# Kernel optimization log

Hardware: AMD Instinct MI355X
Metric: run time of the kernel (lower is better)

## Reference

```python
import jax, jax.numpy as jnp
import numpy as np

B, L, VOCAB = 32768, 512, 50000
CROP_RATIO, MIN_LEN = 0.8, 3
MASK_RATIO, MASK_TOKEN = 0.2, 0
REORDER_RATIO, MIN_W, MAX_W = 0.3, 2, 5


def setup_inputs() -> dict:
    key = jax.random.key(0)
    k1, k2 = jax.random.split(key)
    lens = jax.random.randint(k1, (B,), 1, L + 1)
    items = jax.random.randint(k2, (B, L), 1, VOCAB)
    pos = jnp.arange(L)[None, :]
    item_seq = jnp.where(pos < lens[:, None], items, 0).astype(jnp.int32)
    return {"item_seq": item_seq, "item_seq_len": lens.astype(jnp.int32)}


def _mask_aug(key, seq, lens):
    pos = jnp.arange(seq.shape[1])[None, :]
    valid = (pos < lens[:, None]) & (seq != 0)
    n_valid = valid.sum(axis=1)
    n_mask = jnp.minimum(jnp.maximum(1, (n_valid * MASK_RATIO).astype(jnp.int32)), n_valid)
    scores = jnp.where(valid, jax.random.uniform(key, seq.shape), jnp.inf)
    # rank of each position among valid positions by random score
    rank = jnp.argsort(jnp.argsort(scores, axis=1), axis=1)
    apply_row = (lens > 1) & (n_valid > 0)
    do_mask = valid & (rank < n_mask[:, None]) & apply_row[:, None]
    return jnp.where(do_mask, MASK_TOKEN, seq), lens


def _crop_aug(key, seq, lens):
    Lm = seq.shape[1]
    crop_len = jnp.minimum(jnp.maximum(MIN_LEN, (lens * CROP_RATIO).astype(jnp.int32)), lens)
    max_start = jnp.maximum(lens - crop_len + 1, 1)
    start = (jax.random.uniform(key, (seq.shape[0],)) * max_start).astype(jnp.int32)
    pos = jnp.arange(Lm)[None, :]
    idx = jnp.minimum(start[:, None] + pos, Lm - 1)
    cropped = jnp.where(pos < crop_len[:, None], jnp.take_along_axis(seq, idx, axis=1), 0)
    apply_row = lens > MIN_LEN
    return (jnp.where(apply_row[:, None], cropped, seq),
            jnp.where(apply_row, crop_len, lens))


def _reorder_aug(key, seq, lens):
    Bm, Lm = seq.shape
    k1, k2, k3, k4 = jax.random.split(key, 4)
    pos = jnp.arange(Lm)[None, :]
    valid = (pos < lens[:, None]) & (seq != 0)
    n_valid = valid.sum(axis=1)
    # valid positions first (in order), padding positions after
    valid_idx = jnp.argsort(jnp.where(valid, pos, Lm + pos), axis=1)
    max_w = jnp.minimum(n_valid, MAX_W)
    wsize = MIN_W + (jax.random.uniform(k1, (Bm,)) * jnp.maximum(max_w - MIN_W + 1, 1)).astype(jnp.int32)
    wsize = jnp.clip(wsize, MIN_W, MAX_W)
    max_start = jnp.maximum(n_valid - wsize + 1, 1)
    start = (jax.random.uniform(k2, (Bm,)) * max_start).astype(jnp.int32)
    apply_row = (lens > MIN_W) & (jax.random.uniform(k3, (Bm,)) <= REORDER_RATIO) & (n_valid >= MIN_W)
    k = jnp.arange(MAX_W)[None, :]
    slot_ok = k < wsize[:, None]
    win_cols = jnp.take_along_axis(valid_idx, jnp.minimum(start[:, None] + k, Lm - 1), axis=1)
    win_items = jnp.take_along_axis(seq, win_cols, axis=1)
    # random permutation within the (ragged) window via sorted random keys
    keys = jnp.where(slot_ok, jax.random.uniform(k4, (Bm, MAX_W)), jnp.inf)
    perm = jnp.argsort(keys, axis=1)
    shuffled = jnp.take_along_axis(win_items, perm, axis=1)
    vals = jnp.where(slot_ok & apply_row[:, None], shuffled, win_items)
    rows = jnp.arange(Bm)[:, None]
    return seq.at[rows, win_cols].set(vals), lens


def reference(item_seq, item_seq_len):
    key = jax.random.key(42)
    km, kc, kr = jax.random.split(key, 3)
    mask_seq, mask_len = _mask_aug(km, item_seq, item_seq_len)
    crop_seq, crop_len = _crop_aug(kc, item_seq, item_seq_len)
    reord_seq, reord_len = _reorder_aug(kr, item_seq, item_seq_len)
    return (mask_seq, mask_len, crop_seq, crop_len, reord_seq, reord_len)
```

## Files before the change

kernel.cpp:

```cpp
#include <hip/hip_runtime.h>
#include <stdint.h>


#define NB 32768
#define NL 512
#define NBL (NB * NL)

struct AugKeys {
  uint32_t km0, km1;
  uint32_t kc0, kc1;
  uint32_t r10, r11;
  uint32_t r20, r21;
  uint32_t r30, r31;
  uint32_t r40, r41;
};

__host__ __device__ __forceinline__ uint32_t rotl32(uint32_t x, uint32_t r) {
  return (x << r) | (x >> (32u - r));
}

__host__ __device__ inline void tf2x32(uint32_t k0, uint32_t k1,
                                       uint32_t x0, uint32_t x1,
                                       uint32_t& o0, uint32_t& o1) {
  const uint32_t ks2 = k0 ^ k1 ^ 0x1BD11BDAu;
#define TFR(r) { x0 += x1; x1 = rotl32(x1, r); x1 ^= x0; }
  x0 += k0; x1 += k1;
  TFR(13u) TFR(15u) TFR(26u) TFR(6u)
  x0 += k1; x1 += ks2 + 1u;
  TFR(17u) TFR(29u) TFR(16u) TFR(24u)
  x0 += ks2; x1 += k0 + 2u;
  TFR(13u) TFR(15u) TFR(26u) TFR(6u)
  x0 += k0; x1 += k1 + 3u;
  TFR(17u) TFR(29u) TFR(16u) TFR(24u)
  x0 += k1; x1 += ks2 + 4u;
  TFR(13u) TFR(15u) TFR(26u) TFR(6u)
  x0 += ks2; x1 += k0 + 5u;
#undef TFR
  o0 = x0; o1 = x1;
}

__device__ __forceinline__ float u01f(uint32_t bits) {
  return __uint_as_float((bits >> 9) | 0x3F800000u) - 1.0f;
}

__device__ __forceinline__ uint32_t rbits32(uint32_t k0, uint32_t k1, uint32_t i) {
  uint32_t o0, o1;
  tf2x32(k0, k1, 0u, i, o0, o1);
  return o0 ^ o1;
}

#define SEL8(e, s) \
  (((s) & 4) ? (((s) & 2) ? (((s) & 1) ? e[7] : e[6]) : (((s) & 1) ? e[5] : e[4])) \
             : (((s) & 2) ? (((s) & 1) ? e[3] : e[2]) : (((s) & 1) ? e[1] : e[0])))

__global__ void __launch_bounds__(256)
aug_pipeline(const int* __restrict__ seq, const int* __restrict__ lens,
             int* __restrict__ out, AugKeys K)
{
  __shared__ int s_hist[4][128];
  __shared__ uint32_t s_bin[4][NL];
  __shared__ int s_vb[4][64];
  __shared__ unsigned long long s_D[4][8];
  __shared__ int s_nbin[4];

  const int t = threadIdx.x;
  const int w = t >> 6;
  const int l = t & 63;
  const int b = blockIdx.x * 4 + w;
  const int len = lens[b];
  const int e0 = l * 8;

  const int4 va = reinterpret_cast<const int4*>(seq + (size_t)b * NL)[2 * l];
  const int4 vb = reinterpret_cast<const int4*>(seq + (size_t)b * NL)[2 * l + 1];
  const int elem[8] = {va.x, va.y, va.z, va.w, vb.x, vb.y, vb.z, vb.w};

  float uval = 0.f;
  if (l < 9) {
    uint32_t kk0, kk1, f;
    if (l == 0)      { kk0 = K.kc0; kk1 = K.kc1; f = (uint32_t)b; }
    else if (l == 1) { kk0 = K.r10; kk1 = K.r11; f = (uint32_t)b; }
    else if (l == 2) { kk0 = K.r20; kk1 = K.r21; f = (uint32_t)b; }
    else if (l == 3) { kk0 = K.r30; kk1 = K.r31; f = (uint32_t)b; }
    else             { kk0 = K.r40; kk1 = K.r41; f = (uint32_t)b * 5u + (uint32_t)(l - 4); }
    uval = u01f(rbits32(kk0, kk1, f));
  }
  const float u_c = __shfl(uval, 0);
  const float u_w = __shfl(uval, 1);
  const float u_s = __shfl(uval, 2);
  const float u_a = __shfl(uval, 3);
  float u4[5];
#pragma unroll
  for (int k = 0; k < 5; ++k) u4[k] = __shfl(uval, 4 + k);

  bool val[8];
  int vbyte = 0;
#pragma unroll
  for (int i = 0; i < 8; ++i) {
    val[i] = (e0 + i < len) && (elem[i] != 0);
    vbyte |= (val[i] ? 1 : 0) << i;
  }
  int n_valid = 0;
#pragma unroll
  for (int i = 0; i < 8; ++i) n_valid += (int)__popcll(__ballot(val[i]));

  s_hist[w][2 * l] = 0;
  s_hist[w][2 * l + 1] = 0;
  s_vb[w][l] = vbyte;
  if (l == 0) s_nbin[w] = 0;
  __builtin_amdgcn_wave_barrier();

  uint32_t kk[8];
  uint32_t vsm = 0;
#pragma unroll
  for (int it = 0; it < 8; ++it) {
    if ((it << 6) < len) {
      const int pos = (it << 6) + l;
      const uint32_t bits = rbits32(K.km0, K.km1, (uint32_t)b * NL + (uint32_t)pos);
      kk[it] = (bits & 0xFFFFFE00u) | (uint32_t)pos;
      const int vb8 = s_vb[w][(it << 3) + (l >> 3)];
      const bool vs = (vb8 >> (l & 7)) & 1;
      if (vs) {
        atomicAdd(&s_hist[w][kk[it] >> 25], 1);
        vsm |= 1u << it;
      }
    }
  }
  __builtin_amdgcn_wave_barrier();

  const int h0 = s_hist[w][2 * l];
  const int h1 = s_hist[w][2 * l + 1];
  const int pair = h0 + h1;
  int incl = pair;
#pragma unroll
  for (int d = 1; d < 64; d <<= 1) {
    const int o = __shfl_up(incl, d);
    if (l >= d) incl += o;
  }
  const int ex0 = incl - pair;
  const int ex1 = ex0 + h0;
  const int n_mask = min(max(1, (int)((float)n_valid * 0.2f)), n_valid);
  const bool c0 = (h0 > 0) && (ex0 < n_mask) && (n_mask <= ex0 + h0);
  const bool c1 = (h1 > 0) && (ex1 < n_mask) && (n_mask <= ex1 + h1);
  const unsigned long long B0 = __ballot(c0);
  const unsigned long long B1 = __ballot(c1);
  int tbin = -1, below = 0;
  if (B0) {
    const int tl = __ffsll(B0) - 1;
    tbin = 2 * tl; below = __shfl(ex0, tl);
  } else if (B1) {
    const int tl = __ffsll(B1) - 1;
    tbin = 2 * tl + 1; below = __shfl(ex1, tl);
  }
  const int need = n_mask - below;

#pragma unroll
  for (int it = 0; it < 8; ++it) {
    if ((it << 6) < len) {
      if (((vsm >> it) & 1) && (int)(kk[it] >> 25) == tbin) {
        s_bin[w][atomicAdd(&s_nbin[w], 1)] = kk[it];
      }
    }
  }
  __builtin_amdgcn_wave_barrier();
  const int mtot = s_nbin[w];
  const bool apply_m = (len > 1) && (n_valid > 0);

#pragma unroll
  for (int it = 0; it < 8; ++it) {
    if ((it << 6) < len) {
      int rk = 0;
      for (int j = 0; j < mtot; ++j) rk += (s_bin[w][j] < kk[it]) ? 1 : 0;
      const int bin = (int)(kk[it] >> 25);
      const bool dm = apply_m && ((vsm >> it) & 1) && tbin >= 0 &&
                      (bin < tbin || (bin == tbin && rk < need));
      const unsigned long long Dm = __ballot(dm);
      if (l == 0) s_D[w][it] = Dm;
    }
  }
  __builtin_amdgcn_wave_barrier();

  const unsigned long long Dword = s_D[w][l >> 3];
  const uint32_t dbyte = (uint32_t)(Dword >> (8 * (l & 7))) & 0xFFu;
  int o8[8];
#pragma unroll
  for (int i = 0; i < 8; ++i) {
    o8[i] = (val[i] && ((dbyte >> i) & 1)) ? 0 : elem[i];
  }
  {
    int4* p = reinterpret_cast<int4*>(out + (size_t)b * NL);
    p[2 * l]     = make_int4(o8[0], o8[1], o8[2], o8[3]);
    p[2 * l + 1] = make_int4(o8[4], o8[5], o8[6], o8[7]);
  }

  const int clen = min(max(3, (int)((float)len * 0.8f)), len);
  const int cms = max(len - clen + 1, 1);
  const int cstart = (int)(u_c * (float)cms);
  const bool apply_c = (len > 3);
  int c8[8];
#pragma unroll
  for (int i = 0; i < 8; ++i) {
    const int s = (cstart + i) & 7;
    const int srcl = (cstart + e0 + i) >> 3;
    const int g = __shfl(SEL8(elem, s), srcl);
    c8[i] = apply_c ? ((e0 + i < clen) ? g : 0) : elem[i];
  }
  {
    int4* p = reinterpret_cast<int4*>(out + (size_t)NBL + NB + (size_t)b * NL);
    p[2 * l]     = make_int4(c8[0], c8[1], c8[2], c8[3]);
    p[2 * l + 1] = make_int4(c8[4], c8[5], c8[6], c8[7]);
  }

  const int max_w = min(n_valid, 5);
  int wsize = 2 + (int)(u_w * (float)max(max_w - 1, 1));
  wsize = min(max(wsize, 2), 5);
  const int rms = max(n_valid - wsize + 1, 1);
  const int rstart = (int)(u_s * (float)rms);
  const bool apply_r = (len > 2) && (u_a <= 0.3f) && (n_valid >= 2);

  int cols[5], items[5];
  float fk[5];
#pragma unroll
  for (int k = 0; k < 5; ++k) {
    cols[k] = min(rstart + k, NL - 1);
    const int s = cols[k] & 7;
    items[k] = __shfl(SEL8(elem, s), cols[k] >> 3);
    fk[k] = (k < wsize) ? u4[k] : __int_as_float(0x7F800000);
  }
  int rank5[5];
#pragma unroll
  for (int k = 0; k < 5; ++k) {
    int rr = 0;
#pragma unroll
    for (int j = 0; j < 5; ++j) {
      rr += ((fk[j] < fk[k]) || (fk[j] == fk[k] && j < k)) ? 1 : 0;
    }
    rank5[k] = rr;
  }
  int valk[5];
#pragma unroll
  for (int p = 0; p < 5; ++p) {
    int sh = items[0];
#pragma unroll
    for (int k = 0; k < 5; ++k) if (rank5[k] == p) sh = items[k];
    valk[p] = (apply_r && p < wsize) ? sh : items[p];
  }

  int r8[8] = {elem[0], elem[1], elem[2], elem[3], elem[4], elem[5], elem[6], elem[7]};
#pragma unroll
  for (int k = 0; k < 5; ++k) {
#pragma unroll
    for (int i = 0; i < 8; ++i) if (cols[k] == e0 + i) r8[i] = valk[k];
  }
  {
    int4* p = reinterpret_cast<int4*>(out + 2 * (size_t)NBL + 2 * NB + (size_t)b * NL);
    p[2 * l]     = make_int4(r8[0], r8[1], r8[2], r8[3]);
    p[2 * l + 1] = make_int4(r8[4], r8[5], r8[6], r8[7]);
  }

  if (l == 0) {
    out[(size_t)NBL + b] = len;
    out[2 * (size_t)NBL + NB + b] = apply_c ? clen : len;
    out[3 * (size_t)NBL + 2 * NB + b] = len;
  }
}

extern "C" void kernel_launch(void* const* d_in, const int* in_sizes, int n_in,
                              void* d_out, int out_size, void* d_ws, size_t ws_size,
                              hipStream_t stream) {
  const int* seq  = (const int*)d_in[0];
  const int* lens = (const int*)d_in[1];
  int* out = (int*)d_out;

  AugKeys K;
  uint32_t kr0, kr1;
  tf2x32(0u, 42u, 0u, 0u, K.km0, K.km1);
  tf2x32(0u, 42u, 0u, 1u, K.kc0, K.kc1);
  tf2x32(0u, 42u, 0u, 2u, kr0, kr1);
  tf2x32(kr0, kr1, 0u, 0u, K.r10, K.r11);
  tf2x32(kr0, kr1, 0u, 1u, K.r20, K.r21);
  tf2x32(kr0, kr1, 0u, 2u, K.r30, K.r31);
  tf2x32(kr0, kr1, 0u, 3u, K.r40, K.r41);

  aug_pipeline<<<dim3(NB / 4), dim3(256), 0, stream>>>(seq, lens, out, K);
}
```

Before: 72.48 us.

## Reorder stages, load strided copy for mask path, write mask output directly

Adds a second strided load of each row so the mask validity and output use the same element-per-lane layout as the RNG keys. This removes the shared-memory validity bytes and the ballot/shared mask-bit exchange. The crop and reorder outputs are now written before the mask histogram and selection work, so those stores can overlap with it. The rank loop is restructured to read each shared bin entry once for all eight slots. The cost is reading each input row twice, relying on cache hits, and the mask output is now written with scalar stores instead of int4 stores.

```diff
diff --git a/kernel.cpp b/kernel.cpp
--- a/kernel.cpp
+++ b/kernel.cpp
@@ -59,19 +59,22 @@
 {
   __shared__ int s_hist[4][128];
   __shared__ uint32_t s_bin[4][NL];
-  __shared__ int s_vb[4][64];
-  __shared__ unsigned long long s_D[4][8];
   __shared__ int s_nbin[4];
 
   const int t = threadIdx.x;
   const int w = t >> 6;
   const int l = t & 63;
   const int b = blockIdx.x * 4 + w;
-  const int len = lens[b];
+  const int len = __builtin_amdgcn_readfirstlane(lens[b]);
   const int e0 = l * 8;
-
-  const int4 va = reinterpret_cast<const int4*>(seq + (size_t)b * NL)[2 * l];
-  const int4 vb = reinterpret_cast<const int4*>(seq + (size_t)b * NL)[2 * l + 1];
+  const int* rowp = seq + (size_t)b * NL;
+
+  int es[8];
+#pragma unroll
+  for (int it = 0; it < 8; ++it) es[it] = rowp[(it << 6) + l];
+
+  const int4 va = reinterpret_cast<const int4*>(rowp)[2 * l];
+  const int4 vb = reinterpret_cast<const int4*>(rowp)[2 * l + 1];
   const int elem[8] = {va.x, va.y, va.z, va.w, vb.x, vb.y, vb.z, vb.w};
 
   float uval = 0.f;
@@ -92,37 +95,100 @@
 #pragma unroll
   for (int k = 0; k < 5; ++k) u4[k] = __shfl(uval, 4 + k);
 
-  bool val[8];
-  int vbyte = 0;
-#pragma unroll
-  for (int i = 0; i < 8; ++i) {
-    val[i] = (e0 + i < len) && (elem[i] != 0);
-    vbyte |= (val[i] ? 1 : 0) << i;
-  }
-  int n_valid = 0;
-#pragma unroll
-  for (int i = 0; i < 8; ++i) n_valid += (int)__popcll(__ballot(val[i]));
+  uint32_t vsm = 0;
+  int nv = 0;
+#pragma unroll
+  for (int it = 0; it < 8; ++it) {
+    const bool vs = ((it << 6) + l < len) && (es[it] != 0);
+    vsm |= (uint32_t)vs << it;
+    nv += (int)__popcll(__ballot(vs));
+  }
+  const int n_valid = __builtin_amdgcn_readfirstlane(nv);
+
+  const int clen = min(max(3, (int)((float)len * 0.8f)), len);
+  const int cms = max(len - clen + 1, 1);
+  const int cstart = (int)(u_c * (float)cms);
+  const bool apply_c = (len > 3);
+  {
+    int c8[8];
+#pragma unroll
+    for (int i = 0; i < 8; ++i) {
+      const int s = (cstart + i) & 7;
+      const int srcl = (cstart + e0 + i) >> 3;
+      const int g = __shfl(SEL8(elem, s), srcl);
+      c8[i] = apply_c ? ((e0 + i < clen) ? g : 0) : elem[i];
+    }
+    int4* p = reinterpret_cast<int4*>(out + (size_t)NBL + NB + (size_t)b * NL);
+    p[2 * l]     = make_int4(c8[0], c8[1], c8[2], c8[3]);
+    p[2 * l + 1] = make_int4(c8[4], c8[5], c8[6], c8[7]);
+  }
+
+  if (l == 0) {
+    out[(size_t)NBL + b] = len;
+    out[2 * (size_t)NBL + NB + b] = apply_c ? clen : len;
+    out[3 * (size_t)NBL + 2 * NB + b] = len;
+  }
+
+  {
+    const int max_w = min(n_valid, 5);
+    int wsize = 2 + (int)(u_w * (float)max(max_w - 1, 1));
+    wsize = min(max(wsize, 2), 5);
+    const int rms = max(n_valid - wsize + 1, 1);
+    const int rstart = (int)(u_s * (float)rms);
+    const bool apply_r = (len > 2) && (u_a <= 0.3f) && (n_valid >= 2);
+
+    int cols[5], items[5];
+    float fk[5];
+#pragma unroll
+    for (int k = 0; k < 5; ++k) {
+      cols[k] = min(rstart + k, NL - 1);
+      const int s = cols[k] & 7;
+      items[k] = __shfl(SEL8(elem, s), cols[k] >> 3);
+      fk[k] = (k < wsize) ? u4[k] : __int_as_float(0x7F800000);
+    }
+    int rank5[5];
+#pragma unroll
+    for (int k = 0; k < 5; ++k) {
+      int rr = 0;
+#pragma unroll
+      for (int j = 0; j < 5; ++j) {
+        rr += ((fk[j] < fk[k]) || (fk[j] == fk[k] && j < k)) ? 1 : 0;
+      }
+      rank5[k] = rr;
+    }
+    int valk[5];
+#pragma unroll
+    for (int p = 0; p < 5; ++p) {
+      int sh = items[0];
+#pragma unroll
+      for (int k = 0; k < 5; ++k) if (rank5[k] == p) sh = items[k];
+      valk[p] = (apply_r && p < wsize) ? sh : items[p];
+    }
+
+    int r8[8] = {elem[0], elem[1], elem[2], elem[3], elem[4], elem[5], elem[6], elem[7]};
+#pragma unroll
+    for (int k = 0; k < 5; ++k) {
+#pragma unroll
+      for (int i = 0; i < 8; ++i) if (cols[k] == e0 + i) r8[i] = valk[k];
+    }
+    int4* p = reinterpret_cast<int4*>(out + 2 * (size_t)NBL + 2 * NB + (size_t)b * NL);
+    p[2 * l]     = make_int4(r8[0], r8[1], r8[2], r8[3]);
+    p[2 * l + 1] = make_int4(r8[4], r8[5], r8[6], r8[7]);
+  }
 
   s_hist[w][2 * l] = 0;
   s_hist[w][2 * l + 1] = 0;
-  s_vb[w][l] = vbyte;
   if (l == 0) s_nbin[w] = 0;
   __builtin_amdgcn_wave_barrier();
 
-  uint32_t kk[8];
-  uint32_t vsm = 0;
+  uint32_t kk[8] = {0u, 0u, 0u, 0u, 0u, 0u, 0u, 0u};
 #pragma unroll
   for (int it = 0; it < 8; ++it) {
     if ((it << 6) < len) {
       const int pos = (it << 6) + l;
       const uint32_t bits = rbits32(K.km0, K.km1, (uint32_t)b * NL + (uint32_t)pos);
       kk[it] = (bits & 0xFFFFFE00u) | (uint32_t)pos;
-      const int vb8 = s_vb[w][(it << 3) + (l >> 3)];
-      const bool vs = (vb8 >> (l & 7)) & 1;
-      if (vs) {
-        atomicAdd(&s_hist[w][kk[it] >> 25], 1);
-        vsm |= 1u << it;
-      }
+      if ((vsm >> it) & 1) atomicAdd(&s_hist[w][kk[it] >> 25], 1);
     }
   }
   __builtin_amdgcn_wave_barrier();
@@ -155,112 +221,28 @@
 
 #pragma unroll
   for (int it = 0; it < 8; ++it) {
-    if ((it << 6) < len) {
-      if (((vsm >> it) & 1) && (int)(kk[it] >> 25) == tbin) {
-        s_bin[w][atomicAdd(&s_nbin[w], 1)] = kk[it];
-      }
+    if (((vsm >> it) & 1) && (int)(kk[it] >> 25) == tbin) {
+      s_bin[w][atomicAdd(&s_nbin[w], 1)] = kk[it];
     }
   }
   __builtin_amdgcn_wave_barrier();
   const int mtot = s_nbin[w];
+
+  int rk[8] = {0, 0, 0, 0, 0, 0, 0, 0};
+  for (int j = 0; j < mtot; ++j) {
+    const uint32_t bk = s_bin[w][j];
+#pragma unroll
+    for (int it = 0; it < 8; ++it) rk[it] += (bk < kk[it]) ? 1 : 0;
+  }
+
   const bool apply_m = (len > 1) && (n_valid > 0);
-
-#pragma unroll
-  for (int it = 0; it < 8; ++it) {
-    if ((it << 6) < len) {
-      int rk = 0;
-      for (int j = 0; j < mtot; ++j) rk += (s_bin[w][j] < kk[it]) ? 1 : 0;
-      const int bin = (int)(kk[it] >> 25);
-      const bool dm = apply_m && ((vsm >> it) & 1) && tbin >= 0 &&
-                      (bin < tbin || (bin == tbin && rk < need));
-      const unsigned long long Dm = __ballot(dm);
-      if (l == 0) s_D[w][it] = Dm;
-    }
-  }
-  __builtin_amdgcn_wave_barrier();
-
-  const unsigned long long Dword = s_D[w][l >> 3];
-  const uint32_t dbyte = (uint32_t)(Dword >> (8 * (l & 7))) & 0xFFu;
-  int o8[8];
-#pragma unroll
-  for (int i = 0; i < 8; ++i) {
-    o8[i] = (val[i] && ((dbyte >> i) & 1)) ? 0 : elem[i];
-  }
-  {
-    int4* p = reinterpret_cast<int4*>(out + (size_t)b * NL);
-    p[2 * l]     = make_int4(o8[0], o8[1], o8[2], o8[3]);
-    p[2 * l + 1] = make_int4(o8[4], o8[5], o8[6], o8[7]);
-  }
-
-  const int clen = min(max(3, (int)((float)len * 0.8f)), len);
-  const int cms = max(len - clen + 1, 1);
-  const int cstart = (int)(u_c * (float)cms);
-  const bool apply_c = (len > 3);
-  int c8[8];
-#pragma unroll
-  for (int i = 0; i < 8; ++i) {
-    const int s = (cstart + i) & 7;
-    const int srcl = (cstart + e0 + i) >> 3;
-    const int g = __shfl(SEL8(elem, s), srcl);
-    c8[i] = apply_c ? ((e0 + i < clen) ? g : 0) : elem[i];
-  }
-  {
-    int4* p = reinterpret_cast<int4*>(out + (size_t)NBL + NB + (size_t)b * NL);
-    p[2 * l]     = make_int4(c8[0], c8[1], c8[2], c8[3]);
-    p[2 * l + 1] = make_int4(c8[4], c8[5], c8[6], c8[7]);
-  }
-
-  const int max_w = min(n_valid, 5);
-  int wsize = 2 + (int)(u_w * (float)max(max_w - 1, 1));
-  wsize = min(max(wsize, 2), 5);
-  const int rms = max(n_valid - wsize + 1, 1);
-  const int rstart = (int)(u_s * (float)rms);
-  const bool apply_r = (len > 2) && (u_a <= 0.3f) && (n_valid >= 2);
-
-  int cols[5], items[5];
-  float fk[5];
-#pragma unroll
-  for (int k = 0; k < 5; ++k) {
-    cols[k] = min(rstart + k, NL - 1);
-    const int s = cols[k] & 7;
-    items[k] = __shfl(SEL8(elem, s), cols[k] >> 3);
-    fk[k] = (k < wsize) ? u4[k] : __int_as_float(0x7F800000);
-  }
-  int rank5[5];
-#pragma unroll
-  for (int k = 0; k < 5; ++k) {
-    int rr = 0;
-#pragma unroll
-    for (int j = 0; j < 5; ++j) {
-      rr += ((fk[j] < fk[k]) || (fk[j] == fk[k] && j < k)) ? 1 : 0;
-    }
-    rank5[k] = rr;
-  }
-  int valk[5];
-#pragma unroll
-  for (int p = 0; p < 5; ++p) {
-    int sh = items[0];
-#pragma unroll
-    for (int k = 0; k < 5; ++k) if (rank5[k] == p) sh = items[k];
-    valk[p] = (apply_r && p < wsize) ? sh : items[p];
-  }
-
-  int r8[8] = {elem[0], elem[1], elem[2], elem[3], elem[4], elem[5], elem[6], elem[7]};
-#pragma unroll
-  for (int k = 0; k < 5; ++k) {
-#pragma unroll
-    for (int i = 0; i < 8; ++i) if (cols[k] == e0 + i) r8[i] = valk[k];
-  }
-  {
-    int4* p = reinterpret_cast<int4*>(out + 2 * (size_t)NBL + 2 * NB + (size_t)b * NL);
-    p[2 * l]     = make_int4(r8[0], r8[1], r8[2], r8[3]);
-    p[2 * l + 1] = make_int4(r8[4], r8[5], r8[6], r8[7]);
-  }
-
-  if (l == 0) {
-    out[(size_t)NBL + b] = len;
-    out[2 * (size_t)NBL + NB + b] = apply_c ? clen : len;
-    out[3 * (size_t)NBL + 2 * NB + b] = len;
+  int* mout = out + (size_t)b * NL;
+#pragma unroll
+  for (int it = 0; it < 8; ++it) {
+    const int bin = (int)(kk[it] >> 25);
+    const bool dm = apply_m && ((vsm >> it) & 1) &&
+                    (bin < tbin || (bin == tbin && rk[it] < need));
+    mout[(it << 6) + l] = dm ? 0 : es[it];
   }
 }
 
```

New measurement: 63.53 us. 1.14x faster.
